# Kernel tuning notes

Measured on AMD Instinct MI355X. Metric: run time of the kernel, lower is better.

Reference implementation:

```python
import jax, jax.numpy as jnp
import numpy as np

K = 512
H = 8

def setup_inputs() -> dict:
    key = jax.random.key(0)
    ks = jax.random.split(key, 6)
    b, t, k = 4, 2048, K
    scale = 1.0 / np.sqrt(k)
    return {
        "x": jax.random.normal(ks[0], (b, t, k), dtype=jnp.float32),
        "Wq": jax.random.normal(ks[1], (k, k), dtype=jnp.float32) * scale,
        "Wk": jax.random.normal(ks[2], (k, k), dtype=jnp.float32) * scale,
        "Wv": jax.random.normal(ks[3], (k, k), dtype=jnp.float32) * scale,
        "Wo": jax.random.normal(ks[4], (k, k), dtype=jnp.float32) * scale,
        "bo": jax.random.normal(ks[5], (k,), dtype=jnp.float32) * 0.01,
    }

def reference(x, Wq, Wk, Wv, Wo, bo):
    b, t, k = x.shape
    h = H
    s = k // h
    # nn.Linear: y = x @ W.T ; weights stored [out, in]
    q = (x @ Wq.T).reshape(b, t, h, s)
    kk = (x @ Wk.T).reshape(b, t, h, s)
    v = (x @ Wv.T).reshape(b, t, h, s)
    # scores: note original divides by sqrt(k) (full model dim), not sqrt(s)
    dot = jnp.einsum("bqhs,bkhs->bhqk", q, kk) / jnp.sqrt(jnp.float32(k))
    attn = jax.nn.softmax(dot, axis=-1)
    out = jnp.einsum("bhqk,bkhs->bqhs", attn, v).reshape(b, t, k)
    return out @ Wo.T + bo
```

## Files before the change

### kernel.cpp

```cpp
#include <hip/hip_runtime.h>

typedef _Float16 f16;
typedef _Float16 f16x8 __attribute__((ext_vector_type(8)));
typedef _Float16 f16x4 __attribute__((ext_vector_type(4)));
typedef float    f32x4 __attribute__((ext_vector_type(4)));
typedef __fp16   fp16x2 __attribute__((ext_vector_type(2)));

#define MFMA(a,b,c) __builtin_amdgcn_mfma_f32_16x16x32_f16((a),(b),(c),0,0,0)

#if __has_builtin(__builtin_amdgcn_exp2f)
#define EXP2(x) __builtin_amdgcn_exp2f(x)
#else
#define EXP2(x) exp2f(x)
#endif

__device__ __forceinline__ void gl_lds16(const void* g, void* l) {
  __builtin_amdgcn_global_load_lds(
      (__attribute__((address_space(1))) void*)(void*)(g),
      (__attribute__((address_space(3))) void*)(l),
      16, 0, 0);
}

__device__ __forceinline__ int SWZ(int row) {
  return ((row & 3) | ((row >> 1) & 4)) << 4;
}

__global__ __launch_bounds__(256) void k_convert(
    const float* __restrict__ x, const float* __restrict__ Wq,
    const float* __restrict__ Wk, const float* __restrict__ Wv,
    const float* __restrict__ Wo,
    f16* __restrict__ x_h, f16* __restrict__ wqkv_h, f16* __restrict__ wo_h) {
  const int XQ    = (8192 * 512) / 4;
  const int WQKVQ = (1536 * 512) / 4;
  const int WOQ   = (512 * 512) / 4;
  const int total = XQ + WQKVQ + WOQ;
  for (int q = blockIdx.x * blockDim.x + threadIdx.x; q < total;
       q += gridDim.x * blockDim.x) {
    const float* src;
    f16* dst;
    if (q < XQ) {
      src = x + q * 4;
      dst = x_h + q * 4;
    } else if (q < XQ + WQKVQ) {
      int j  = q - XQ;
      int r  = j >> 7;
      int c0 = (j & 127) * 4;
      const float* w = (r < 512) ? Wq : (r < 1024) ? Wk : Wv;
      src = w + (r & 511) * 512 + c0;
      dst = wqkv_h + j * 4;
    } else {
      int j = q - XQ - WQKVQ;
      src = Wo + j * 4;
      dst = wo_h + j * 4;
    }
    float4 v = *(const float4*)src;
    f16x4 o = {(f16)v.x, (f16)v.y, (f16)v.z, (f16)v.w};
    *(f16x4*)dst = o;
  }
}

__device__ __forceinline__ void gemm_core(const f16* __restrict__ A,
                                          const f16* __restrict__ B,
                                          int bm, int bn, f32x4 (&acc)[4][4],
                                          char* smem) {
  f16* As = (f16*)smem;
  f16* Bs = (f16*)(smem + 32768);
  const int tid  = threadIdx.x;
  const int lane = tid & 63;
  const int w    = tid >> 6;
  const int wr   = (w >> 1) & 1, wc = w & 1;
  const int r0   = tid >> 3;
  const int cb   = (tid & 7) << 4;

  auto stage = [&](int buf, int kt) {
#pragma unroll
    for (int inst = 0; inst < 4; ++inst) {
      const int row  = inst * 32 + r0;
      const int csrc = cb ^ ((row & 7) << 4);
      gl_lds16(A + (bm + row) * 512 + kt + (csrc >> 1),
               (char*)As + buf * 16384 + inst * 4096 + w * 1024);
      gl_lds16(B + (bn + row) * 512 + kt + (csrc >> 1),
               (char*)Bs + buf * 16384 + inst * 4096 + w * 1024);
    }
  };

  stage(0, 0);
#pragma unroll
  for (int t = 0; t < 8; ++t) {
    const int cur = t & 1;
    asm volatile("s_waitcnt vmcnt(0)" ::: "memory");
    __builtin_amdgcn_s_barrier();
    __builtin_amdgcn_sched_barrier(0);
    if (t < 7) stage(cur ^ 1, (t + 1) * 64);
    f16x8 af[4][2], bf[4][2];
#pragma unroll
    for (int i = 0; i < 4; ++i) {
      const int ra = wr * 64 + i * 16 + (lane & 15);
      const int rb = wc * 64 + i * 16 + (lane & 15);
#pragma unroll
      for (int ks = 0; ks < 2; ++ks) {
        const int cc = ks * 64 + ((lane >> 4) << 4);
        af[i][ks] = *(const f16x8*)((const char*)As + cur * 16384 + ra * 128 + (cc ^ ((ra & 7) << 4)));
        bf[i][ks] = *(const f16x8*)((const char*)Bs + cur * 16384 + rb * 128 + (cc ^ ((rb & 7) << 4)));
      }
    }
    __builtin_amdgcn_s_setprio(1);
#pragma unroll
    for (int i = 0; i < 4; ++i)
#pragma unroll
      for (int j = 0; j < 4; ++j) {
        acc[i][j] = MFMA(af[i][0], bf[j][0], acc[i][j]);
        acc[i][j] = MFMA(af[i][1], bf[j][1], acc[i][j]);
      }
    __builtin_amdgcn_s_setprio(0);
  }
}

__global__ __launch_bounds__(256) void k_gemm_qkv(
    const f16* __restrict__ A, const f16* __restrict__ B,
    f16* __restrict__ q_h, f16* __restrict__ k_h, f16* __restrict__ vt_h) {
  __shared__ char smem[65536];
  const int wgid = blockIdx.x;
  const int nw   = (wgid & 7) * 96 + (wgid >> 3);
  const int bm   = (nw / 12) * 128;
  const int bn   = (nw % 12) * 128;
  const bool isV = (bn >= 1024);

  f32x4 acc[4][4] = {};
  if (isV) gemm_core(B, A, bn, bm, acc, smem);
  else     gemm_core(A, B, bm, bn, acc, smem);

  const int tid  = threadIdx.x;
  const int lane = tid & 63;
  const int w    = tid >> 6;
  const int wr   = (w >> 1) & 1, wc = w & 1;
  const float qscale = (bn < 512) ? 0.044194173824159216f * 1.4426950408889634f : 1.0f;

  __syncthreads();
  f16* T = (f16*)smem;
#pragma unroll
  for (int i = 0; i < 4; ++i) {
    const int rr = wr * 64 + i * 16 + ((lane >> 4) << 2);
#pragma unroll
    for (int j = 0; j < 4; ++j) {
      const int cc = wc * 64 + j * 16 + (lane & 15);
#pragma unroll
      for (int r = 0; r < 4; ++r)
        T[(rr + r) * 136 + cc] = (f16)(acc[i][j][r] * qscale);
    }
  }
  __syncthreads();

  f16* dst_qk = (bn < 512) ? q_h : k_h;
#pragma unroll
  for (int k = 0; k < 8; ++k) {
    const int idx  = k * 256 + tid;
    const int row  = idx >> 4;
    const int col8 = (idx & 15) * 8;
    const f16x8 v = *(const f16x8*)(T + row * 136 + col8);
    if (!isV) {
      const int m = bm + row, b = m >> 11, t = m & 2047;
      const int nn = (bn + col8) & 511, h = nn >> 6, s = nn & 63;
      *(f16x8*)(dst_qk + ((size_t)((b * 8 + h) * 2048 + t)) * 64 + s) = v;
    } else {
      const int nn = (bn - 1024) + row, h = nn >> 6, s = nn & 63;
      const int m = bm + col8, b = m >> 11, t = m & 2047;
      *(f16x8*)(vt_h + ((size_t)((b * 8 + h) * 64 + s)) * 2048 + t) = v;
    }
  }
}

__global__ __launch_bounds__(512, 2) void k_attn(
    const f16* __restrict__ q_h, const f16* __restrict__ k_h,
    const f16* __restrict__ vt_h, f16* __restrict__ a_h) {
  __shared__ char smem[65536];

  const int tid  = threadIdx.x;
  const int lane = tid & 63;
  const int w    = tid >> 6;
  const int g    = w >> 2;
  const int wg   = w & 3;

  int id = blockIdx.x;
  id = (id & 7) * 32 + (id >> 3);
  const int qt = (id & 7) * 256;
  const int bh = id >> 3;

  const f16* qb = q_h + (size_t)bh * 2048 * 64;
  const f16* kb = k_h + (size_t)bh * 2048 * 64;
  const f16* vb = vt_h + (size_t)bh * 64 * 2048;

  auto KsP = [&](int grp, int buf) { return smem + grp * 32768 + buf * 16384; };
  auto VsP = [&](int grp, int buf) { return smem + grp * 32768 + buf * 16384 + 8192; };

  const int m  = lane & 15;
  const int hi = lane >> 4;

  f16x8 qf[4][2];
#pragma unroll
  for (int i = 0; i < 4; ++i) {
    const int qrow = qt + wg * 64 + i * 16 + m;
#pragma unroll
    for (int ks = 0; ks < 2; ++ks)
      qf[i][ks] = *(const f16x8*)(qb + qrow * 64 + ks * 32 + hi * 8);
  }

  f32x4 oacc[4][4] = {};
  f32x4 lrun[4]    = {};

  const int gt  = tid & 255;
  const int r0  = gt >> 3;
  const int cbb = (tid & 7) << 4;

  const f16 one = (f16)1.0f;
  const f16x8 ones = {one, one, one, one, one, one, one, one};

  auto stage = [&](int buf, int t) {
    const int ktv = g * 1024 + t * 64;
#pragma unroll
    for (int inst = 0; inst < 2; ++inst) {
      const int row  = inst * 32 + r0;
      const int csrc = cbb ^ SWZ(row);
      gl_lds16(kb + (ktv + row) * 64 + (csrc >> 1),
               KsP(g, buf) + inst * 4096 + wg * 1024);
      gl_lds16(vb + row * 2048 + ktv + (csrc >> 1),
               VsP(g, buf) + inst * 4096 + wg * 1024);
    }
  };

  auto pack4 = [](float a, float b, float c, float d) -> unsigned long long {
    union { fp16x2 h2[2]; unsigned long long u; } t;
    t.h2[0] = __builtin_amdgcn_cvt_pkrtz(a, b);
    t.h2[1] = __builtin_amdgcn_cvt_pkrtz(c, d);
    return t.u;
  };

  auto tile = [&](const char* ksb, const char* vsb) {
    f16x8 kf[4][2];
#pragma unroll
    for (int n = 0; n < 4; ++n) {
      const int row = ((n >> 1) << 5) + ((m >> 2) << 3) + ((n & 1) << 2) + (m & 3);
      const int sw  = SWZ(row);
#pragma unroll
      for (int ks = 0; ks < 2; ++ks) {
        const int c = (ks * 64 + (hi << 4)) ^ sw;
        kf[n][ks] = *(const f16x8*)(ksb + row * 128 + c);
      }
    }
    f32x4 sf[4][4];
    __builtin_amdgcn_s_setprio(1);
#pragma unroll
    for (int i = 0; i < 4; ++i)
#pragma unroll
      for (int n = 0; n < 4; ++n) {
        f32x4 s = {0.f, 0.f, 0.f, 0.f};
        s = MFMA(kf[n][0], qf[i][0], s);
        s = MFMA(kf[n][1], qf[i][1], s);
        sf[i][n] = s;
      }
    __builtin_amdgcn_s_setprio(0);
    f16x8 pa[4][2];
#pragma unroll
    for (int i = 0; i < 4; ++i)
#pragma unroll
      for (int ks = 0; ks < 2; ++ks) {
        union { unsigned long long u[2]; f16x8 v; } u;
        u.u[0] = pack4(EXP2(sf[i][2 * ks][0]), EXP2(sf[i][2 * ks][1]),
                       EXP2(sf[i][2 * ks][2]), EXP2(sf[i][2 * ks][3]));
        u.u[1] = pack4(EXP2(sf[i][2 * ks + 1][0]), EXP2(sf[i][2 * ks + 1][1]),
                       EXP2(sf[i][2 * ks + 1][2]), EXP2(sf[i][2 * ks + 1][3]));
        pa[i][ks] = u.v;
      }
    __builtin_amdgcn_s_setprio(1);
#pragma unroll
    for (int i = 0; i < 4; ++i) {
      lrun[i] = MFMA(pa[i][0], ones, lrun[i]);
      lrun[i] = MFMA(pa[i][1], ones, lrun[i]);
    }
#pragma unroll
    for (int n = 0; n < 4; ++n) {
      const int row = n * 16 + m;
      const int sw  = SWZ(row);
      const f16x8 vf0 = *(const f16x8*)(vsb + row * 128 + ((hi << 4) ^ sw));
      const f16x8 vf1 = *(const f16x8*)(vsb + row * 128 + ((64 + (hi << 4)) ^ sw));
#pragma unroll
      for (int i = 0; i < 4; ++i) {
        oacc[i][n] = MFMA(pa[i][0], vf0, oacc[i][n]);
        oacc[i][n] = MFMA(pa[i][1], vf1, oacc[i][n]);
      }
    }
    __builtin_amdgcn_s_setprio(0);
  };

  stage(0, 0);
  for (int j = 0; j < 16; ++j) {
    const int cur = j & 1;
    asm volatile("s_waitcnt vmcnt(0)" ::: "memory");
    __builtin_amdgcn_s_barrier();
    __builtin_amdgcn_sched_barrier(0);
    if (j < 15) stage(cur ^ 1, j + 1);
    tile(KsP(g, cur), VsP(g, cur));
  }

  __syncthreads();
  float* Ol = (float*)smem;
  float* l1 = (float*)(smem + 34816);

  const int b2 = bh >> 3, h2 = bh & 7;
#pragma unroll
  for (int p = 0; p < 2; ++p) {
    if (g == 1 && (wg >> 1) == p) {
#pragma unroll
      for (int i = 0; i < 4; ++i)
#pragma unroll
        for (int r = 0; r < 4; ++r) {
          const int ql = (wg * 64 + i * 16 + hi * 4 + r) & 127;
#pragma unroll
          for (int n = 0; n < 4; ++n)
            Ol[ql * 68 + n * 16 + m] = oacc[i][n][r];
          if (m == 0) l1[ql] = lrun[i][r];
        }
    }
    __syncthreads();
    if (g == 0 && (wg >> 1) == p) {
#pragma unroll
      for (int i = 0; i < 4; ++i)
#pragma unroll
        for (int r = 0; r < 4; ++r) {
          const int qg = wg * 64 + i * 16 + hi * 4 + r;
          const int ql = qg & 127;
          const float rl = 1.0f / (lrun[i][r] + l1[ql]);
          const int qrow = qt + qg;
#pragma unroll
          for (int n = 0; n < 4; ++n) {
            const int s = n * 16 + m;
            const float o = oacc[i][n][r] + Ol[ql * 68 + s];
            a_h[(size_t)(b2 * 2048 + qrow) * 512 + h2 * 64 + s] = (f16)(o * rl);
          }
        }
    }
    __syncthreads();
  }
}

__global__ __launch_bounds__(256) void k_gemm_out(
    const f16* __restrict__ A, const f16* __restrict__ B,
    const float* __restrict__ bo, float* __restrict__ out) {
  __shared__ char smem[65536];
  const int wgid = blockIdx.x;
  const int nw   = (wgid & 7) * 32 + (wgid >> 3);
  const int bm   = (nw >> 2) * 128;
  const int bn   = (nw & 3) * 128;
  f32x4 acc[4][4] = {};
  gemm_core(A, B, bm, bn, acc, smem);

  const int tid  = threadIdx.x;
  const int lane = tid & 63;
  const int w    = tid >> 6;
  const int wr   = (w >> 1) & 1, wc = w & 1;
#pragma unroll
  for (int i = 0; i < 4; ++i) {
    const int m0 = bm + wr * 64 + i * 16 + ((lane >> 4) << 2);
#pragma unroll
    for (int j = 0; j < 4; ++j) {
      const int n = bn + wc * 64 + j * 16 + (lane & 15);
      const float bias = bo[n];
#pragma unroll
      for (int r = 0; r < 4; ++r)
        __builtin_nontemporal_store(acc[i][j][r] + bias,
                                    &out[(size_t)(m0 + r) * 512 + n]);
    }
  }
}

extern "C" void kernel_launch(void* const* d_in, const int* in_sizes, int n_in,
                              void* d_out, int out_size, void* d_ws, size_t ws_size,
                              hipStream_t stream) {
  const float* x  = (const float*)d_in[0];
  const float* Wq = (const float*)d_in[1];
  const float* Wk = (const float*)d_in[2];
  const float* Wv = (const float*)d_in[3];
  const float* Wo = (const float*)d_in[4];
  const float* bo = (const float*)d_in[5];
  float* out = (float*)d_out;

  char* ws = (char*)d_ws;
  f16* x_h    = (f16*)(ws);
  f16* wqkv_h = (f16*)(ws + 8388608);
  f16* wo_h   = (f16*)(ws + 9961472);
  f16* q_h    = (f16*)(ws + 10485760);
  f16* k_h    = (f16*)(ws + 18874368);
  f16* vt_h   = (f16*)(ws + 27262976);
  f16* a_h    = (f16*)(ws + 35651584);
  (void)ws_size; (void)in_sizes; (void)n_in; (void)out_size;

  k_convert<<<2048, 256, 0, stream>>>(x, Wq, Wk, Wv, Wo, x_h, wqkv_h, wo_h);
  k_gemm_qkv<<<768, 256, 0, stream>>>(x_h, wqkv_h, q_h, k_h, vt_h);
  k_attn<<<256, 512, 0, stream>>>(q_h, k_h, vt_h, a_h);
  k_gemm_out<<<256, 256, 0, stream>>>(a_h, wo_h, bo, out);
}
```

Baseline: 80.75 us.

## Use 64x128 output tiles in out-projection GEMM with dedicated double-buffered loop

Replaces the shared 128x128 gemm_core call in the output projection with a custom 64x128 tile kernel. It uses double-buffered LDS staging via global_load_lds with XOR swizzle, and each wave computes a 64x32 slice. The grid doubles to 512 workgroups, so more of the GPU's compute units are busy for this small GEMM. In exchange, B tiles get less reuse per workgroup and more tiles are loaded redundantly.

```diff
diff --git a/kernel.cpp b/kernel.cpp
--- a/kernel.cpp
+++ b/kernel.cpp
@@ -346,24 +346,83 @@
 __global__ __launch_bounds__(256) void k_gemm_out(
     const f16* __restrict__ A, const f16* __restrict__ B,
     const float* __restrict__ bo, float* __restrict__ out) {
-  __shared__ char smem[65536];
+  __shared__ char smem[49152];
+  f16* As = (f16*)smem;
+  f16* Bs = (f16*)(smem + 16384);
+
   const int wgid = blockIdx.x;
-  const int nw   = (wgid & 7) * 32 + (wgid >> 3);
-  const int bm   = (nw >> 2) * 128;
+  const int nw   = (wgid & 7) * 64 + (wgid >> 3);
+  const int bm   = (nw >> 2) * 64;
   const int bn   = (nw & 3) * 128;
-  f32x4 acc[4][4] = {};
-  gemm_core(A, B, bm, bn, acc, smem);
 
   const int tid  = threadIdx.x;
   const int lane = tid & 63;
   const int w    = tid >> 6;
-  const int wr   = (w >> 1) & 1, wc = w & 1;
+  const int r0   = tid >> 3;
+  const int cb   = (tid & 7) << 4;
+
+  auto stage = [&](int buf, int kt) {
+#pragma unroll
+    for (int inst = 0; inst < 2; ++inst) {
+      const int row  = inst * 32 + r0;
+      const int csrc = cb ^ ((row & 7) << 4);
+      gl_lds16(A + (size_t)(bm + row) * 512 + kt + (csrc >> 1),
+               (char*)As + buf * 8192 + inst * 4096 + w * 1024);
+    }
+#pragma unroll
+    for (int inst = 0; inst < 4; ++inst) {
+      const int row  = inst * 32 + r0;
+      const int csrc = cb ^ ((row & 7) << 4);
+      gl_lds16(B + (size_t)(bn + row) * 512 + kt + (csrc >> 1),
+               (char*)Bs + buf * 16384 + inst * 4096 + w * 1024);
+    }
+  };
+
+  f32x4 acc[4][2] = {};
+  stage(0, 0);
+#pragma unroll
+  for (int t = 0; t < 8; ++t) {
+    const int cur = t & 1;
+    asm volatile("s_waitcnt vmcnt(0)" ::: "memory");
+    __builtin_amdgcn_s_barrier();
+    __builtin_amdgcn_sched_barrier(0);
+    if (t < 7) stage(cur ^ 1, (t + 1) * 64);
+    f16x8 af[4][2], bf[2][2];
+#pragma unroll
+    for (int i = 0; i < 4; ++i) {
+      const int ra = i * 16 + (lane & 15);
+#pragma unroll
+      for (int ks = 0; ks < 2; ++ks) {
+        const int cc = ks * 64 + ((lane >> 4) << 4);
+        af[i][ks] = *(const f16x8*)((const char*)As + cur * 8192 + ra * 128 + (cc ^ ((ra & 7) << 4)));
+      }
+    }
+#pragma unroll
+    for (int j = 0; j < 2; ++j) {
+      const int rb = w * 32 + j * 16 + (lane & 15);
+#pragma unroll
+      for (int ks = 0; ks < 2; ++ks) {
+        const int cc = ks * 64 + ((lane >> 4) << 4);
+        bf[j][ks] = *(const f16x8*)((const char*)Bs + cur * 16384 + rb * 128 + (cc ^ ((rb & 7) << 4)));
+      }
+    }
+    __builtin_amdgcn_s_setprio(1);
+#pragma unroll
+    for (int i = 0; i < 4; ++i)
+#pragma unroll
+      for (int j = 0; j < 2; ++j) {
+        acc[i][j] = MFMA(af[i][0], bf[j][0], acc[i][j]);
+        acc[i][j] = MFMA(af[i][1], bf[j][1], acc[i][j]);
+      }
+    __builtin_amdgcn_s_setprio(0);
+  }
+
 #pragma unroll
   for (int i = 0; i < 4; ++i) {
-    const int m0 = bm + wr * 64 + i * 16 + ((lane >> 4) << 2);
-#pragma unroll
-    for (int j = 0; j < 4; ++j) {
-      const int n = bn + wc * 64 + j * 16 + (lane & 15);
+    const int m0 = bm + i * 16 + ((lane >> 4) << 2);
+#pragma unroll
+    for (int j = 0; j < 2; ++j) {
+      const int n = bn + w * 32 + j * 16 + (lane & 15);
       const float bias = bo[n];
 #pragma unroll
       for (int r = 0; r < 4; ++r)
@@ -397,5 +456,5 @@
   k_convert<<<2048, 256, 0, stream>>>(x, Wq, Wk, Wv, Wo, x_h, wqkv_h, wo_h);
   k_gemm_qkv<<<768, 256, 0, stream>>>(x_h, wqkv_h, q_h, k_h, vt_h);
   k_attn<<<256, 512, 0, stream>>>(q_h, k_h, vt_h, a_h);
-  k_gemm_out<<<256, 256, 0, stream>>>(a_h, wo_h, bo, out);
-}
+  k_gemm_out<<<512, 256, 0, stream>>>(a_h, wo_h, bo, out);
+}
```

New measurement: 80.61 us. Within noise of the previous version (-0.2%).
